# Performance work log

Hardware: AMD Instinct MI355X
Metric: run time of the kernel (lower is better)

The kernel has to match this reference:

```python
import jax, jax.numpy as jnp
import numpy as np

B, S, D = 4, 2048, 1024
H, HD = 16, 64  # n_heads, head_dim; D == H*HD


def setup_inputs() -> dict:
    key = jax.random.key(0)
    k1, k2, k3, k4, k5 = jax.random.split(key, 5)
    s = 0.02
    return {
        "x": jax.random.normal(k1, (B, S, D), dtype=jnp.float32),
        "w_qkv": jax.random.normal(k2, (D, 3 * D), dtype=jnp.float32) * s,
        "b_qkv": jax.random.normal(k3, (3 * D,), dtype=jnp.float32) * s,
        "w_out": jax.random.normal(k4, (D, D), dtype=jnp.float32) * s,
        "b_out": jax.random.normal(k5, (D,), dtype=jnp.float32) * s,
    }


def reference(x, w_qkv, b_qkv, w_out, b_out):
    b, s, d = x.shape
    qkv = x @ w_qkv + b_qkv                      # [B,S,3D]
    qkv = qkv.reshape(b, s, 3, H, HD)
    qkv = jnp.transpose(qkv, (2, 0, 3, 1, 4))    # [3,B,H,S,HD]
    q, k, v = qkv[0], qkv[1], qkv[2]
    scale = 1.0 / np.sqrt(HD).astype(np.float32)
    scores = jnp.einsum("bhqd,bhkd->bhqk", q, k) * scale  # [B,H,S,S]
    causal = jnp.tril(jnp.ones((s, s), dtype=bool))
    scores = jnp.where(causal[None, None], scores, -jnp.inf)
    weights = jax.nn.softmax(scores, axis=-1)
    attn = jnp.einsum("bhqk,bhkd->bhqd", weights, v)       # [B,H,S,HD]
    attn = jnp.transpose(attn, (0, 2, 1, 3)).reshape(b, s, d)
    return attn @ w_out + b_out
```

## Files before the change

kernel.cpp:

```cpp
#include <hip/hip_runtime.h>
#include <hip/hip_bf16.h>

#define B_DIM 4
#define S_DIM 2048
#define D_DIM 1024
#define H_DIM 16
#define HD_DIM 64

using bf16 = __hip_bfloat16;
using bf16x8 = __attribute__((ext_vector_type(8))) short;
using f32x4 = __attribute__((ext_vector_type(4))) float;

__device__ inline unsigned short f2bfu(float f) {
    bf16 h = __float2bfloat16(f);
    unsigned short s;
    __builtin_memcpy(&s, &h, 2);
    return s;
}
__device__ inline unsigned int pack2bf(float a, float b) {
    return (unsigned int)f2bfu(a) | ((unsigned int)f2bfu(b) << 16);
}

typedef __attribute__((address_space(1))) const void cg_void;
typedef __attribute__((address_space(3))) void lds_void;
__device__ inline void gload_lds16(const void* g, void* l) {
    __builtin_amdgcn_global_load_lds((cg_void*)g, (lds_void*)l, 16, 0, 0);
}

__global__ __launch_bounds__(256) void conv_bf16_kernel(const float* __restrict__ in,
                                                        bf16* __restrict__ out, int n4) {
    int i = blockIdx.x * 256 + threadIdx.x;
    if (i >= n4) return;
    float4 v = reinterpret_cast<const float4*>(in)[i];
    ushort4 o;
    o.x = f2bfu(v.x); o.y = f2bfu(v.y); o.z = f2bfu(v.z); o.w = f2bfu(v.w);
    reinterpret_cast<ushort4*>(out)[i] = o;
}

__global__ __launch_bounds__(256) void transpose_bf16_kernel(const float* __restrict__ in,
                                                             bf16* __restrict__ out,
                                                             int R, int C) {
    __shared__ float tile[32][33];
    int c0 = blockIdx.x * 32, r0 = blockIdx.y * 32;
    int tx = threadIdx.x, ty = threadIdx.y;
#pragma unroll
    for (int i = 0; i < 32; i += 8)
        tile[ty + i][tx] = in[(size_t)(r0 + ty + i) * C + c0 + tx];
    __syncthreads();
#pragma unroll
    for (int i = 0; i < 32; i += 8)
        out[(size_t)(c0 + ty + i) * R + r0 + tx] = __float2bfloat16(tile[tx][ty + i]);
}

#define GEMM_PREAMBLE()                                                        \
    const int K = D_DIM;                                                       \
    __shared__ __align__(16) char smem[65536];                                 \
    int m0 = blockIdx.y * 128;                                                 \
    int n0 = blockIdx.x * 128;                                                 \
    int tid = threadIdx.x;                                                     \
    int lane = tid & 63;                                                       \
    int w = tid >> 6;                                                          \
    int wr = w >> 1, wc = w & 1;                                               \
    int lr = lane & 15, lk = lane >> 4;                                        \
    f32x4 acc[4][4] = {};                                                      \
    int sr8 = lane >> 3;                                     \
    int scol = (((lane & 7) * 16) ^ (sr8 << 4)) >> 1;    \
    int wub = w * 1024;                                                        \
    const int rsw = (lr & 7) << 4;                                             \
    const bf16* Arow = A + (size_t)(m0 + w * 8 + sr8) * K + scol;              \
    const bf16* Brow = BT + (size_t)(n0 + w * 8 + sr8) * K + scol;

#define GEMM_STAGE(buf, kk)                                                    \
    do {                                                                       \
        char* ab_ = smem + (buf) * 32768;                                      \
        gload_lds16(Arow + (kk), ab_ + wub);                                   \
        gload_lds16(Arow + 32 * 1024 + (kk), ab_ + 4096 + wub);                \
        gload_lds16(Arow + 64 * 1024 + (kk), ab_ + 8192 + wub);                \
        gload_lds16(Arow + 96 * 1024 + (kk), ab_ + 12288 + wub);               \
        gload_lds16(Brow + (kk), ab_ + 16384 + wub);                           \
        gload_lds16(Brow + 32 * 1024 + (kk), ab_ + 20480 + wub);               \
        gload_lds16(Brow + 64 * 1024 + (kk), ab_ + 24576 + wub);               \
        gload_lds16(Brow + 96 * 1024 + (kk), ab_ + 28672 + wub);               \
    } while (0)

#define GEMM_MAINLOOP()                                                        \
    const int NT = K / 64;                                             \
    GEMM_STAGE(0, 0);                                                          \
    for (int t = 0; t < NT; ++t) {                                             \
        asm volatile("s_waitcnt vmcnt(0)" ::: "memory");                       \
        __builtin_amdgcn_s_barrier();                                          \
        __builtin_amdgcn_sched_barrier(0);                                     \
        if (t + 1 < NT) GEMM_STAGE((t + 1) & 1, (t + 1) * 64);                 \
        char* as = smem + (t & 1) * 32768;                                     \
        char* bs = as + 16384;                                                 \
        bf16x8 af[4][2], bfr[4][2];                                            \
        _Pragma("unroll")                                                      \
        for (int m = 0; m < 4; ++m) {                                          \
            int rb = (wr * 64 + m * 16 + lr) * 128;                            \
            af[m][0] = *(const bf16x8*)(as + rb + ((lk * 16) ^ rsw));          \
            af[m][1] = *(const bf16x8*)(as + rb + ((64 + lk * 16) ^ rsw));     \
        }                                                                      \
        _Pragma("unroll")                                                      \
        for (int n = 0; n < 4; ++n) {                                          \
            int rb = (wc * 64 + n * 16 + lr) * 128;                            \
            bfr[n][0] = *(const bf16x8*)(bs + rb + ((lk * 16) ^ rsw));         \
            bfr[n][1] = *(const bf16x8*)(bs + rb + ((64 + lk * 16) ^ rsw));    \
        }                                                                      \
        __builtin_amdgcn_s_setprio(1);                                         \
        _Pragma("unroll")                                                      \
        for (int m = 0; m < 4; ++m)                                            \
            _Pragma("unroll")                                                  \
            for (int n = 0; n < 4; ++n) {                                      \
                acc[m][n] = __builtin_amdgcn_mfma_f32_16x16x32_bf16(           \
                    af[m][0], bfr[n][0], acc[m][n], 0, 0, 0);                  \
                acc[m][n] = __builtin_amdgcn_mfma_f32_16x16x32_bf16(           \
                    af[m][1], bfr[n][1], acc[m][n], 0, 0, 0);                  \
            }                                                                  \
        __builtin_amdgcn_s_setprio(0);                                         \
    }

__global__ __launch_bounds__(256, 2) void gemm_qkv_kernel(const bf16* __restrict__ A,
                                                          const bf16* __restrict__ BT,
                                                          const float* __restrict__ bias,
                                                          bf16* __restrict__ Qo,
                                                          bf16* __restrict__ Ko,
                                                          bf16* __restrict__ Vt) {
    GEMM_PREAMBLE();
    GEMM_MAINLOOP();
    const float QS = 0.18033688f;
    int third = n0 >> 10;
#pragma unroll
    for (int m = 0; m < 4; ++m) {
        int row = m0 + wr * 64 + m * 16 + lk * 4;
        int b = row >> 11, s = row & 2047;
#pragma unroll
        for (int n = 0; n < 4; ++n) {
            int col = n0 + wc * 64 + n * 16 + lr;
            int rem = col & 1023;
            int h = rem >> 6, hd = rem & 63;
            float bv = bias[col];
            if (third == 0) {
#pragma unroll
                for (int i = 0; i < 4; ++i)
                    Qo[(((size_t)b * H_DIM + h) * S_DIM + s + i) * HD_DIM + hd] =
                        __float2bfloat16((acc[m][n][i] + bv) * QS);
            } else if (third == 1) {
#pragma unroll
                for (int i = 0; i < 4; ++i)
                    Ko[(((size_t)b * H_DIM + h) * S_DIM + s + i) * HD_DIM + hd] =
                        __float2bfloat16(acc[m][n][i] + bv);
            } else {
                uint2 d;
                d.x = pack2bf(acc[m][n][0] + bv, acc[m][n][1] + bv);
                d.y = pack2bf(acc[m][n][2] + bv, acc[m][n][3] + bv);
                *(uint2*)&Vt[(((size_t)b * H_DIM + h) * HD_DIM + hd) * S_DIM + s] = d;
            }
        }
    }
}

__global__ __launch_bounds__(256, 4) void attn_kernel(const bf16* __restrict__ Q,
                                                      const bf16* __restrict__ K,
                                                      const bf16* __restrict__ Vt,
                                                      bf16* __restrict__ Aout) {
    __shared__ __align__(16) char smem[40960];
    int bid = blockIdx.x;
    int bh = bid & 63;
    int st = 15 - (bid >> 6);
    int b = bh >> 4, h = bh & 15;
    int w = threadIdx.x >> 6;
    int lane = threadIdx.x & 63;
    int lr = lane & 15, lk = lane >> 4;

    const short* Qs = (const short*)(Q + (size_t)bh * S_DIM * HD_DIM);
    const short* Ks = (const short*)(K + (size_t)bh * S_DIM * HD_DIM);
    const short* Vs = (const short*)(Vt + (size_t)bh * HD_DIM * S_DIM);
    char* pb = smem + 32768 + w * 2048;
    const int sw = (lr & 7) << 4;

    int srow = w * 8 + (lane >> 3);
    int sblk = ((lane & 7) ^ (lane >> 3)) * 8;
    int wub = w * 1024;

    int q0w = st * 128 + w * 32;
    int nt = 2 * st + 2;

    bf16x8 qf[2][2];
#pragma unroll
    for (int qg = 0; qg < 2; ++qg)
#pragma unroll
        for (int c = 0; c < 2; ++c)
            qf[qg][c] = *(const bf16x8*)&Qs[(size_t)(q0w + qg * 16 + lr) * 64 + c * 32 + lk * 8];

    bf16x8 onesv;
#pragma unroll
    for (int z = 0; z < 8; ++z) onesv[z] = (short)0x3F80;

    f32x4 o[4][2] = {};
    f32x4 ol[2] = {};

    gload_lds16(Ks + (size_t)srow * 64 + sblk, smem + wub);
    gload_lds16(Ks + (size_t)(32 + srow) * 64 + sblk, smem + 4096 + wub);
    gload_lds16(Vs + (size_t)srow * S_DIM + sblk, smem + 16384 + wub);
    gload_lds16(Vs + (size_t)(32 + srow) * S_DIM + sblk, smem + 20480 + wub);

    for (int t = 0; t < nt; ++t) {
        int cur = t & 1;
        int kv0 = t * 64;
        __syncthreads();
        if (t + 1 < nt) {
            int kn = kv0 + 64;
            char* kd = smem + (cur ^ 1) * 8192;
            char* vd = smem + 16384 + (cur ^ 1) * 8192;
            gload_lds16(Ks + (size_t)(kn + srow) * 64 + sblk, kd + wub);
            gload_lds16(Ks + (size_t)(kn + 32 + srow) * 64 + sblk, kd + 4096 + wub);
            gload_lds16(Vs + (size_t)srow * S_DIM + kn + sblk, vd + wub);
            gload_lds16(Vs + (size_t)(32 + srow) * S_DIM + kn + sblk, vd + 4096 + wub);
        }
        char* kt = smem + cur * 8192;
        char* vt = smem + 16384 + cur * 8192;

        f32x4 s[4][2] = {};
        __builtin_amdgcn_s_setprio(1);
#pragma unroll
        for (int m = 0; m < 4; ++m) {
            int rb = (m * 16 + lr) * 128;
            bf16x8 ka = *(const bf16x8*)(kt + rb + ((lk * 16) ^ sw));
            bf16x8 kb2 = *(const bf16x8*)(kt + rb + ((64 + lk * 16) ^ sw));
            s[m][0] = __builtin_amdgcn_mfma_f32_16x16x32_bf16(ka, qf[0][0], s[m][0], 0, 0, 0);
            s[m][0] = __builtin_amdgcn_mfma_f32_16x16x32_bf16(kb2, qf[0][1], s[m][0], 0, 0, 0);
            s[m][1] = __builtin_amdgcn_mfma_f32_16x16x32_bf16(ka, qf[1][0], s[m][1], 0, 0, 0);
            s[m][1] = __builtin_amdgcn_mfma_f32_16x16x32_bf16(kb2, qf[1][1], s[m][1], 0, 0, 0);
        }
        __builtin_amdgcn_s_setprio(0);

        if (kv0 + 63 > q0w) {
#pragma unroll
            for (int m = 0; m < 4; ++m)
#pragma unroll
                for (int qg = 0; qg < 2; ++qg) {
                    int qq = q0w + qg * 16 + lr;
#pragma unroll
                    for (int i = 0; i < 4; ++i)
                        if (kv0 + m * 16 + lk * 4 + i > qq) s[m][qg][i] = -1e30f;
                }
        }

#pragma unroll
        for (int m = 0; m < 4; ++m)
#pragma unroll
            for (int qg = 0; qg < 2; ++qg)
#pragma unroll
                for (int i = 0; i < 4; ++i) s[m][qg][i] = exp2f(s[m][qg][i]);

        bf16x8 pf[2][2];
#pragma unroll
        for (int qg = 0; qg < 2; ++qg) {
#pragma unroll
            for (int m = 0; m < 4; ++m) {
                uint2 d;
                d.x = pack2bf(s[m][qg][0], s[m][qg][1]);
                d.y = pack2bf(s[m][qg][2], s[m][qg][3]);
                *(uint2*)(pb + lr * 128 + ((m * 32 + lk * 8) ^ sw)) = d;
            }
            pf[qg][0] = *(const bf16x8*)(pb + lr * 128 + ((lk * 16) ^ sw));
            pf[qg][1] = *(const bf16x8*)(pb + lr * 128 + ((64 + lk * 16) ^ sw));
        }

        __builtin_amdgcn_s_setprio(1);
#pragma unroll
        for (int m = 0; m < 4; ++m) {
            int rb = (m * 16 + lr) * 128;
            bf16x8 va = *(const bf16x8*)(vt + rb + ((lk * 16) ^ sw));
            bf16x8 vb2 = *(const bf16x8*)(vt + rb + ((64 + lk * 16) ^ sw));
            o[m][0] = __builtin_amdgcn_mfma_f32_16x16x32_bf16(va, pf[0][0], o[m][0], 0, 0, 0);
            o[m][0] = __builtin_amdgcn_mfma_f32_16x16x32_bf16(vb2, pf[0][1], o[m][0], 0, 0, 0);
            o[m][1] = __builtin_amdgcn_mfma_f32_16x16x32_bf16(va, pf[1][0], o[m][1], 0, 0, 0);
            o[m][1] = __builtin_amdgcn_mfma_f32_16x16x32_bf16(vb2, pf[1][1], o[m][1], 0, 0, 0);
        }
        ol[0] = __builtin_amdgcn_mfma_f32_16x16x32_bf16(onesv, pf[0][0], ol[0], 0, 0, 0);
        ol[0] = __builtin_amdgcn_mfma_f32_16x16x32_bf16(onesv, pf[0][1], ol[0], 0, 0, 0);
        ol[1] = __builtin_amdgcn_mfma_f32_16x16x32_bf16(onesv, pf[1][0], ol[1], 0, 0, 0);
        ol[1] = __builtin_amdgcn_mfma_f32_16x16x32_bf16(onesv, pf[1][1], ol[1], 0, 0, 0);
        __builtin_amdgcn_s_setprio(0);
    }

    short* op = (short*)Aout;
#pragma unroll
    for (int qg = 0; qg < 2; ++qg) {
        float inv = 1.0f / ol[qg][0];
        size_t orow = ((size_t)b * S_DIM + q0w + qg * 16 + lr) * D_DIM + h * 64;
#pragma unroll
        for (int m = 0; m < 4; ++m) {
            uint2 d;
            d.x = pack2bf(o[m][qg][0] * inv, o[m][qg][1] * inv);
            d.y = pack2bf(o[m][qg][2] * inv, o[m][qg][3] * inv);
            *(uint2*)(op + orow + m * 16 + lk * 4) = d;
        }
    }
}

__global__ __launch_bounds__(256, 2) void gemm_out_kernel(const bf16* __restrict__ A,
                                                          const bf16* __restrict__ BT,
                                                          const float* __restrict__ bias,
                                                          float* __restrict__ Out) {
    GEMM_PREAMBLE();
    GEMM_MAINLOOP();
#pragma unroll
    for (int m = 0; m < 4; ++m) {
        int row = m0 + wr * 64 + m * 16 + lk * 4;
#pragma unroll
        for (int n = 0; n < 4; ++n) {
            int col = n0 + wc * 64 + n * 16 + lr;
            float bv = bias[col];
#pragma unroll
            for (int i = 0; i < 4; ++i)
                Out[(size_t)(row + i) * D_DIM + col] = acc[m][n][i] + bv;
        }
    }
}

extern "C" void kernel_launch(void* const* d_in, const int* in_sizes, int n_in,
                              void* d_out, int out_size, void* d_ws, size_t ws_size,
                              hipStream_t stream) {
    const float* x = (const float*)d_in[0];
    const float* w_qkv = (const float*)d_in[1];
    const float* b_qkv = (const float*)d_in[2];
    const float* w_out = (const float*)d_in[3];
    const float* b_out = (const float*)d_in[4];
    float* out = (float*)d_out;

    char* ws = (char*)d_ws;
    const size_t SZ_X = (size_t)B_DIM * S_DIM * D_DIM * 2;
    const size_t SZ_WQKV = (size_t)D_DIM * 3 * D_DIM * 2;
    const size_t SZ_WOUT = (size_t)D_DIM * D_DIM * 2;
    bf16* xb = (bf16*)(ws);
    bf16* wqkvT = (bf16*)(ws + SZ_X);
    bf16* woutT = (bf16*)(ws + SZ_X + SZ_WQKV);
    bf16* Qb = (bf16*)(ws + SZ_X + SZ_WQKV + SZ_WOUT);
    bf16* Kb = (bf16*)(ws + SZ_X + SZ_WQKV + SZ_WOUT + SZ_X);
    bf16* Vtb = (bf16*)(ws + SZ_X + SZ_WQKV + SZ_WOUT + 2 * SZ_X);

    {
        int n4 = (B_DIM * S_DIM * D_DIM) / 4;
        conv_bf16_kernel<<<n4 / 256, 256, 0, stream>>>(x, xb, n4);
    }
    transpose_bf16_kernel<<<dim3(3 * D_DIM / 32, D_DIM / 32), dim3(32, 8), 0, stream>>>(
        w_qkv, wqkvT, D_DIM, 3 * D_DIM);
    transpose_bf16_kernel<<<dim3(D_DIM / 32, D_DIM / 32), dim3(32, 8), 0, stream>>>(
        w_out, woutT, D_DIM, D_DIM);
    gemm_qkv_kernel<<<dim3(3 * D_DIM / 128, B_DIM * S_DIM / 128), 256, 0, stream>>>(
        xb, wqkvT, b_qkv, Qb, Kb, Vtb);
    attn_kernel<<<dim3(B_DIM * H_DIM * 16), 256, 0, stream>>>(Qb, Kb, Vtb, xb);
    gemm_out_kernel<<<dim3(D_DIM / 128, B_DIM * S_DIM / 128), 256, 0, stream>>>(
        xb, woutT, b_out, out);
}
```

Baseline: 160.6 us.

## Pair causal q-tiles per block and use 8 waves of 16 query rows

The attention kernel now launches half as many 512-thread blocks. Each block handles two query tiles (st and 15-st) in sequence, which balances the causal work across blocks. Each wave owns 16 query rows instead of 32, and a wave skips KV tiles past its own diagonal, computing only the needed m-blocks on the diagonal tile. This cuts wasted masked MFMA work and load imbalance, at the cost of less register reuse of K/V fragments per wave, wasted LDS loads for waves that skip, and possible occupancy changes from the larger block size.

```diff
diff --git a/kernel.cpp b/kernel.cpp
--- a/kernel.cpp
+++ b/kernel.cpp
@@ -159,17 +159,18 @@
     }
 }
 
-__global__ __launch_bounds__(256, 4) void attn_kernel(const bf16* __restrict__ Q,
+__global__ __launch_bounds__(512, 4) void attn_kernel(const bf16* __restrict__ Q,
                                                       const bf16* __restrict__ K,
                                                       const bf16* __restrict__ Vt,
                                                       bf16* __restrict__ Aout) {
-    __shared__ __align__(16) char smem[40960];
+    __shared__ __align__(16) char smem[49152];
     int bid = blockIdx.x;
     int bh = bid & 63;
-    int st = 15 - (bid >> 6);
+    int pr = bid >> 6;
     int b = bh >> 4, h = bh & 15;
-    int w = threadIdx.x >> 6;
-    int lane = threadIdx.x & 63;
+    int tid = threadIdx.x;
+    int w = tid >> 6;
+    int lane = tid & 63;
     int lr = lane & 15, lk = lane >> 4;
 
     const short* Qs = (const short*)(Q + (size_t)bh * S_DIM * HD_DIM);
@@ -178,123 +179,117 @@
     char* pb = smem + 32768 + w * 2048;
     const int sw = (lr & 7) << 4;
 
-    int srow = w * 8 + (lane >> 3);
-    int sblk = ((lane & 7) ^ (lane >> 3)) * 8;
+    int srow = tid >> 3;
+    int sblk = ((tid & 7) ^ (srow & 7)) * 8;
     int wub = w * 1024;
 
-    int q0w = st * 128 + w * 32;
-    int nt = 2 * st + 2;
-
-    bf16x8 qf[2][2];
-#pragma unroll
-    for (int qg = 0; qg < 2; ++qg)
+    bf16x8 onesv;
+#pragma unroll
+    for (int z = 0; z < 8; ++z) onesv[z] = (short)0x3F80;
+    short* op = (short*)Aout;
+
+    for (int it = 0; it < 2; ++it) {
+        int st = it ? pr : (15 - pr);
+        int q0w = st * 128 + w * 16;
+        int nt = 2 * st + 2;
+        int twl = 2 * st + (w >> 2);
+
+        bf16x8 qf[2];
 #pragma unroll
         for (int c = 0; c < 2; ++c)
-            qf[qg][c] = *(const bf16x8*)&Qs[(size_t)(q0w + qg * 16 + lr) * 64 + c * 32 + lk * 8];
-
-    bf16x8 onesv;
-#pragma unroll
-    for (int z = 0; z < 8; ++z) onesv[z] = (short)0x3F80;
-
-    f32x4 o[4][2] = {};
-    f32x4 ol[2] = {};
-
-    gload_lds16(Ks + (size_t)srow * 64 + sblk, smem + wub);
-    gload_lds16(Ks + (size_t)(32 + srow) * 64 + sblk, smem + 4096 + wub);
-    gload_lds16(Vs + (size_t)srow * S_DIM + sblk, smem + 16384 + wub);
-    gload_lds16(Vs + (size_t)(32 + srow) * S_DIM + sblk, smem + 20480 + wub);
-
-    for (int t = 0; t < nt; ++t) {
-        int cur = t & 1;
-        int kv0 = t * 64;
+            qf[c] = *(const bf16x8*)&Qs[(size_t)(q0w + lr) * 64 + c * 32 + lk * 8];
+
+        f32x4 o[4] = {};
+        f32x4 ol = {};
+
         __syncthreads();
-        if (t + 1 < nt) {
-            int kn = kv0 + 64;
-            char* kd = smem + (cur ^ 1) * 8192;
-            char* vd = smem + 16384 + (cur ^ 1) * 8192;
-            gload_lds16(Ks + (size_t)(kn + srow) * 64 + sblk, kd + wub);
-            gload_lds16(Ks + (size_t)(kn + 32 + srow) * 64 + sblk, kd + 4096 + wub);
-            gload_lds16(Vs + (size_t)srow * S_DIM + kn + sblk, vd + wub);
-            gload_lds16(Vs + (size_t)(32 + srow) * S_DIM + kn + sblk, vd + 4096 + wub);
-        }
-        char* kt = smem + cur * 8192;
-        char* vt = smem + 16384 + cur * 8192;
-
-        f32x4 s[4][2] = {};
-        __builtin_amdgcn_s_setprio(1);
-#pragma unroll
-        for (int m = 0; m < 4; ++m) {
-            int rb = (m * 16 + lr) * 128;
-            bf16x8 ka = *(const bf16x8*)(kt + rb + ((lk * 16) ^ sw));
-            bf16x8 kb2 = *(const bf16x8*)(kt + rb + ((64 + lk * 16) ^ sw));
-            s[m][0] = __builtin_amdgcn_mfma_f32_16x16x32_bf16(ka, qf[0][0], s[m][0], 0, 0, 0);
-            s[m][0] = __builtin_amdgcn_mfma_f32_16x16x32_bf16(kb2, qf[0][1], s[m][0], 0, 0, 0);
-            s[m][1] = __builtin_amdgcn_mfma_f32_16x16x32_bf16(ka, qf[1][0], s[m][1], 0, 0, 0);
-            s[m][1] = __builtin_amdgcn_mfma_f32_16x16x32_bf16(kb2, qf[1][1], s[m][1], 0, 0, 0);
-        }
-        __builtin_amdgcn_s_setprio(0);
-
-        if (kv0 + 63 > q0w) {
+        gload_lds16(Ks + (size_t)srow * 64 + sblk, smem + wub);
+        gload_lds16(Vs + (size_t)srow * S_DIM + sblk, smem + 16384 + wub);
+
+        for (int t = 0; t < nt; ++t) {
+            int cur = t & 1;
+            int kv0 = t * 64;
+            __syncthreads();
+            if (t + 1 < nt) {
+                int kn = kv0 + 64;
+                gload_lds16(Ks + (size_t)(kn + srow) * 64 + sblk,
+                            smem + (cur ^ 1) * 8192 + wub);
+                gload_lds16(Vs + (size_t)srow * S_DIM + kn + sblk,
+                            smem + 16384 + (cur ^ 1) * 8192 + wub);
+            }
+            if (t > twl) continue;
+            char* kt = smem + cur * 8192;
+            char* vt = smem + 16384 + cur * 8192;
+            bool diag = (t == twl);
+
+            f32x4 s[4] = {};
+            __builtin_amdgcn_s_setprio(1);
+            if (!diag) {
+#pragma unroll
+                for (int m = 0; m < 4; ++m) {
+                    int rb = (m * 16 + lr) * 128;
+                    bf16x8 ka = *(const bf16x8*)(kt + rb + ((lk * 16) ^ sw));
+                    bf16x8 kb2 = *(const bf16x8*)(kt + rb + ((64 + lk * 16) ^ sw));
+                    s[m] = __builtin_amdgcn_mfma_f32_16x16x32_bf16(ka, qf[0], s[m], 0, 0, 0);
+                    s[m] = __builtin_amdgcn_mfma_f32_16x16x32_bf16(kb2, qf[1], s[m], 0, 0, 0);
+                }
+            } else {
+                int mhi = (w & 3) + 1;
+                for (int m = 0; m < mhi; ++m) {
+                    int rb = (m * 16 + lr) * 128;
+                    bf16x8 ka = *(const bf16x8*)(kt + rb + ((lk * 16) ^ sw));
+                    bf16x8 kb2 = *(const bf16x8*)(kt + rb + ((64 + lk * 16) ^ sw));
+                    s[m] = __builtin_amdgcn_mfma_f32_16x16x32_bf16(ka, qf[0], s[m], 0, 0, 0);
+                    s[m] = __builtin_amdgcn_mfma_f32_16x16x32_bf16(kb2, qf[1], s[m], 0, 0, 0);
+                }
+            }
+            __builtin_amdgcn_s_setprio(0);
+
+            if (diag) {
+                int qq = 16 * (w & 3) + lr;
+#pragma unroll
+                for (int m = 0; m < 4; ++m)
+#pragma unroll
+                    for (int i = 0; i < 4; ++i)
+                        if (m * 16 + lk * 4 + i > qq) s[m][i] = -1e30f;
+            }
+
 #pragma unroll
             for (int m = 0; m < 4; ++m)
 #pragma unroll
-                for (int qg = 0; qg < 2; ++qg) {
-                    int qq = q0w + qg * 16 + lr;
-#pragma unroll
-                    for (int i = 0; i < 4; ++i)
-                        if (kv0 + m * 16 + lk * 4 + i > qq) s[m][qg][i] = -1e30f;
-                }
-        }
-
-#pragma unroll
-        for (int m = 0; m < 4; ++m)
-#pragma unroll
-            for (int qg = 0; qg < 2; ++qg)
-#pragma unroll
-                for (int i = 0; i < 4; ++i) s[m][qg][i] = exp2f(s[m][qg][i]);
-
-        bf16x8 pf[2][2];
-#pragma unroll
-        for (int qg = 0; qg < 2; ++qg) {
+                for (int i = 0; i < 4; ++i) s[m][i] = exp2f(s[m][i]);
+
 #pragma unroll
             for (int m = 0; m < 4; ++m) {
                 uint2 d;
-                d.x = pack2bf(s[m][qg][0], s[m][qg][1]);
-                d.y = pack2bf(s[m][qg][2], s[m][qg][3]);
+                d.x = pack2bf(s[m][0], s[m][1]);
+                d.y = pack2bf(s[m][2], s[m][3]);
                 *(uint2*)(pb + lr * 128 + ((m * 32 + lk * 8) ^ sw)) = d;
             }
-            pf[qg][0] = *(const bf16x8*)(pb + lr * 128 + ((lk * 16) ^ sw));
-            pf[qg][1] = *(const bf16x8*)(pb + lr * 128 + ((64 + lk * 16) ^ sw));
+            bf16x8 pf0 = *(const bf16x8*)(pb + lr * 128 + ((lk * 16) ^ sw));
+            bf16x8 pf1 = *(const bf16x8*)(pb + lr * 128 + ((64 + lk * 16) ^ sw));
+
+            __builtin_amdgcn_s_setprio(1);
+#pragma unroll
+            for (int m = 0; m < 4; ++m) {
+                int rb = (m * 16 + lr) * 128;
+                bf16x8 va = *(const bf16x8*)(vt + rb + ((lk * 16) ^ sw));
+                bf16x8 vb2 = *(const bf16x8*)(vt + rb + ((64 + lk * 16) ^ sw));
+                o[m] = __builtin_amdgcn_mfma_f32_16x16x32_bf16(va, pf0, o[m], 0, 0, 0);
+                o[m] = __builtin_amdgcn_mfma_f32_16x16x32_bf16(vb2, pf1, o[m], 0, 0, 0);
+            }
+            ol = __builtin_amdgcn_mfma_f32_16x16x32_bf16(onesv, pf0, ol, 0, 0, 0);
+            ol = __builtin_amdgcn_mfma_f32_16x16x32_bf16(onesv, pf1, ol, 0, 0, 0);
+            __builtin_amdgcn_s_setprio(0);
         }
 
-        __builtin_amdgcn_s_setprio(1);
-#pragma unroll
-        for (int m = 0; m < 4; ++m) {
-            int rb = (m * 16 + lr) * 128;
-            bf16x8 va = *(const bf16x8*)(vt + rb + ((lk * 16) ^ sw));
-            bf16x8 vb2 = *(const bf16x8*)(vt + rb + ((64 + lk * 16) ^ sw));
-            o[m][0] = __builtin_amdgcn_mfma_f32_16x16x32_bf16(va, pf[0][0], o[m][0], 0, 0, 0);
-            o[m][0] = __builtin_amdgcn_mfma_f32_16x16x32_bf16(vb2, pf[0][1], o[m][0], 0, 0, 0);
-            o[m][1] = __builtin_amdgcn_mfma_f32_16x16x32_bf16(va, pf[1][0], o[m][1], 0, 0, 0);
-            o[m][1] = __builtin_amdgcn_mfma_f32_16x16x32_bf16(vb2, pf[1][1], o[m][1], 0, 0, 0);
-        }
-        ol[0] = __builtin_amdgcn_mfma_f32_16x16x32_bf16(onesv, pf[0][0], ol[0], 0, 0, 0);
-        ol[0] = __builtin_amdgcn_mfma_f32_16x16x32_bf16(onesv, pf[0][1], ol[0], 0, 0, 0);
-        ol[1] = __builtin_amdgcn_mfma_f32_16x16x32_bf16(onesv, pf[1][0], ol[1], 0, 0, 0);
-        ol[1] = __builtin_amdgcn_mfma_f32_16x16x32_bf16(onesv, pf[1][1], ol[1], 0, 0, 0);
-        __builtin_amdgcn_s_setprio(0);
-    }
-
-    short* op = (short*)Aout;
-#pragma unroll
-    for (int qg = 0; qg < 2; ++qg) {
-        float inv = 1.0f / ol[qg][0];
-        size_t orow = ((size_t)b * S_DIM + q0w + qg * 16 + lr) * D_DIM + h * 64;
+        float inv = 1.0f / ol[0];
+        size_t orow = ((size_t)b * S_DIM + q0w + lr) * D_DIM + h * 64;
 #pragma unroll
         for (int m = 0; m < 4; ++m) {
             uint2 d;
-            d.x = pack2bf(o[m][qg][0] * inv, o[m][qg][1] * inv);
-            d.y = pack2bf(o[m][qg][2] * inv, o[m][qg][3] * inv);
+            d.x = pack2bf(o[m][0] * inv, o[m][1] * inv);
+            d.y = pack2bf(o[m][2] * inv, o[m][3] * inv);
             *(uint2*)(op + orow + m * 16 + lk * 4) = d;
         }
     }
@@ -351,7 +346,7 @@
         w_out, woutT, D_DIM, D_DIM);
     gemm_qkv_kernel<<<dim3(3 * D_DIM / 128, B_DIM * S_DIM / 128), 256, 0, stream>>>(
         xb, wqkvT, b_qkv, Qb, Kb, Vtb);
-    attn_kernel<<<dim3(B_DIM * H_DIM * 16), 256, 0, stream>>>(Qb, Kb, Vtb, xb);
+    attn_kernel<<<dim3(B_DIM * H_DIM * 8), 512, 0, stream>>>(Qb, Kb, Vtb, xb);
     gemm_out_kernel<<<dim3(D_DIM / 128, B_DIM * S_DIM / 128), 256, 0, stream>>>(
         xb, woutT, b_out, out);
 }
```

New measurement: 159.5 us. No clear change (-0.7%).
